# Kernel tuning notes

Measured on AMD Instinct MI355X. Metric: run time of the kernel, lower is better.

Reference implementation:

```python
import jax, jax.numpy as jnp
import numpy as np
from jax import lax

MAX_U = 5
MAX_V = 5
BN_EPS = 1e-5


def _conv(x, w, b, p):
    # NCHW conv with symmetric padding p (torch Conv2d padding=p)
    y = lax.conv_general_dilated(x, w, (1, 1), [(p, p), (p, p)],
                                 dimension_numbers=('NCHW', 'OIHW', 'NCHW'))
    return y + b[None, :, None, None]


def _branch(x, w3, b3, w5, b5, w7, b7):
    a3 = jax.nn.relu(_conv(x, w3, b3, 1))
    a5 = jax.nn.relu(_conv(jnp.concatenate([a3, x], 1), w5, b5, 2))
    a7 = jax.nn.relu(_conv(jnp.concatenate([a5, x], 1), w7, b7, 3))
    return jnp.concatenate([a3, a5, a7], 1)  # [B, 448, H, W]


def _dct_basis(n, kmax, dtype):
    # orthonormal DCT-II basis rows for frequencies u < kmax: [kmax, n]
    i = jnp.arange(n, dtype=dtype)
    u = jnp.arange(kmax, dtype=dtype)
    basis = jnp.cos(jnp.pi * (2.0 * i[None, :] + 1.0) * u[:, None] / (2.0 * n))
    scale = jnp.where(u == 0, jnp.sqrt(1.0 / n), jnp.sqrt(2.0 / n))
    return basis * scale[:, None]


def setup_inputs() -> dict:
    key = jax.random.key(0)
    ks = iter(jax.random.split(key, 64))

    def w(shape, s=0.05):
        return (jax.random.normal(next(ks), shape, jnp.float32) * s)

    cin = 3  # input_channels per group (x has 2*cin = 6 channels)
    inp = {"x": jax.random.normal(next(ks), (16, 6, 64, 64), jnp.float32)}
    for g in (1, 2):
        for b in (1, 2):
            inp[f"g{g}b{b}c3_w"] = w((64, cin, 3, 3))
            inp[f"g{g}b{b}c3_b"] = w((64,))
            inp[f"g{g}b{b}c5_w"] = w((128, 64 + cin, 5, 5))
            inp[f"g{g}b{b}c5_b"] = w((128,))
            inp[f"g{g}b{b}c7_w"] = w((256, 128 + cin, 7, 7))
            inp[f"g{g}b{b}c7_b"] = w((256,))
    inp["gap_w"] = w((12, 1792)); inp["gap_b"] = w((12,))
    inp["dct_w"] = w((12, 1792)); inp["dct_b"] = w((12,))
    inp["bn_gamma"] = jnp.ones((1792,), jnp.float32)
    inp["bn_beta"] = jnp.zeros((1792,), jnp.float32)
    inp["bn_mean"] = jnp.zeros((1792,), jnp.float32)
    inp["bn_var"] = jnp.ones((1792,), jnp.float32)
    return inp


def reference(x,
              g1b1c3_w, g1b1c3_b, g1b1c5_w, g1b1c5_b, g1b1c7_w, g1b1c7_b,
              g1b2c3_w, g1b2c3_b, g1b2c5_w, g1b2c5_b, g1b2c7_w, g1b2c7_b,
              g2b1c3_w, g2b1c3_b, g2b1c5_w, g2b1c5_b, g2b1c7_w, g2b1c7_b,
              g2b2c3_w, g2b2c3_b, g2b2c5_w, g2b2c5_b, g2b2c7_w, g2b2c7_b,
              gap_w, gap_b, dct_w, dct_b, bn_gamma, bn_beta, bn_mean, bn_var):
    B, C, H, W = x.shape  # C is even (6)
    half = C // 2
    x1, x2 = x[:, :half], x[:, half:]
    out1 = jnp.concatenate([
        _branch(x1, g1b1c3_w, g1b1c3_b, g1b1c5_w, g1b1c5_b, g1b1c7_w, g1b1c7_b),
        _branch(x1, g1b2c3_w, g1b2c3_b, g1b2c5_w, g1b2c5_b, g1b2c7_w, g1b2c7_b)], 1)
    out2 = jnp.concatenate([
        _branch(x2, g2b1c3_w, g2b1c3_b, g2b1c5_w, g2b1c5_b, g2b1c7_w, g2b1c7_b),
        _branch(x2, g2b2c3_w, g2b2c3_b, g2b2c5_w, g2b2c5_b, g2b2c7_w, g2b2c7_b)], 1)
    concat_out = jnp.concatenate([out1, out2], 1)  # [B, 1792, H, W]

    # GAP head
    gap = concat_out.mean((2, 3))  # [B, 1792]
    gap_pred = gap @ gap_w.T + gap_b

    # Batched multi-frequency DCT compression: low-frequency 5x5 block of the
    # 2D DCT-II of each channel, averaged -> one scalar per channel.
    Bh = _dct_basis(H, MAX_U, x.dtype)  # [5, H]
    Bw = _dct_basis(W, MAX_V, x.dtype)  # [5, W]
    coeff = jnp.einsum('bchw,uh,vw->bcuv', concat_out, Bh, Bw)  # [B,1792,5,5]
    dct_feat = coeff.mean((2, 3))  # [B, 1792]

    # BatchNorm1d (inference with running stats); dropout is identity in eval.
    bn = bn_gamma * (dct_feat - bn_mean) / jnp.sqrt(bn_var + BN_EPS) + bn_beta
    dct_pred = bn @ dct_w.T + dct_b
    return gap_pred, dct_pred
```

## Files before the change

kernel.cpp:

```cpp
#include <hip/hip_runtime.h>
#include <hip/hip_bf16.h>
#include <math.h>

#define HW 64
#define NPIX 4096
#define NB 16
#define NCH 1792
#define PW 72
#define PROWS 70
#define PLANE (PROWS * PW)

typedef __bf16 bf16;
typedef __bf16 bf16x8 __attribute__((ext_vector_type(8)));
typedef float f32x4 __attribute__((ext_vector_type(4)));

struct PtrQuad { const float* p[4]; };

constexpr size_t W3SZ = 9 * 1 * 64 * 32;
constexpr size_t W5SZ = 25 * 3 * 128 * 32;
constexpr size_t W7SZ = 49 * 5 * 256 * 32;
constexpr size_t WBR  = W3SZ + W5SZ + W7SZ;
constexpr size_t PLE  = (size_t)PLANE * 8;

__global__ __launch_bounds__(256) void init_kernel(float* __restrict__ gap_sum,
                                                   float* __restrict__ dct_sum,
                                                   float* __restrict__ dctw) {
    int tid = blockIdx.x * 256 + threadIdx.x;
    if (tid < NB * NCH) { gap_sum[tid] = 0.f; dct_sum[tid] = 0.f; }
    if (blockIdx.x == 0 && threadIdx.x < HW) {
        int i = threadIdx.x;
        float s = 0.f;
        for (int u = 0; u < 5; ++u) {
            float scale = (u == 0) ? 0.125f : 0.17677669529663687f;
            s += cosf(3.14159265358979323846f * (2.f * i + 1.f) * u / 128.f) * scale;
        }
        dctw[i] = s * 0.2f;
    }
}

__global__ __launch_bounds__(256) void zero_kernel(float4* __restrict__ p, long n) {
    long i = (long)blockIdx.x * 256 + threadIdx.x;
    long stride = (long)gridDim.x * 256;
    for (; i < n; i += stride) p[i] = float4{0.f, 0.f, 0.f, 0.f};
}

__global__ __launch_bounds__(256) void prep_x_kernel(const float* __restrict__ x,
                                                     bf16* __restrict__ xp) {
    int tid = blockIdx.x * 256 + threadIdx.x;
    if (tid >= NB * 2 * NPIX) return;
    int pix = tid & (NPIX - 1);
    int g = (tid >> 12) & 1;
    int b = tid >> 13;
    int h = pix >> 6, w = pix & 63;
    size_t base = ((size_t)(b * 2 + g) * 4) * PLE + ((size_t)(h + 3) * PW + (w + 3)) * 8;
    for (int c = 0; c < 3; ++c)
        xp[base + c] = (bf16)x[((size_t)(b * 6 + g * 3 + c)) * NPIX + pix];
}

template <int K, int CHUNKS, int CIN_ACT, int COUT>
__global__ __launch_bounds__(256) void prep_w_all(PtrQuad src, bf16* __restrict__ dst) {
    constexpr int CIN = CIN_ACT + 3;
    constexpr int TOT = K * K * CHUNKS * COUT * 32;
    int tid = blockIdx.x * 256 + threadIdx.x;
    if (tid >= 4 * TOT) return;
    int br = tid / TOT;
    int idx = tid - br * TOT;
    int cc = idx & 31;
    int co = (idx >> 5) % COUT;
    int rest = idx / (32 * COUT);
    int chunk = rest % CHUNKS;
    int ks = rest / CHUNKS;
    int ky = ks / K, kx = ks % K;
    int ci;
    if (chunk < CHUNKS - 1) ci = chunk * 32 + cc;
    else ci = (cc < 3) ? (CIN_ACT + cc) : -1;
    const float* w = src.p[br];
    float v = (ci >= 0) ? w[(((size_t)co * CIN + ci) * K + ky) * K + kx] : 0.f;
    dst[(size_t)br * WBR + idx] = (bf16)v;
}

template <int K, int CHUNKS, int COUT, int NBLK, bool STORE>
__global__ __launch_bounds__(512, 2) void conv_mfma(
    const bf16* __restrict__ act_in,
    const bf16* __restrict__ xpad,
    const bf16* __restrict__ wall, size_t stage_woff,
    PtrQuad biasq,
    bf16* __restrict__ act_out,
    float* __restrict__ gap_sum, float* __restrict__ dct_sum,
    int stage_coff, const float* __restrict__ dctw, int br0)
{
    constexpr int PAD = K / 2;
    constexpr int COFF = 3 - PAD;
    constexpr int HR = 8 + K - 1;
    constexpr int RH = HR / 2;
    constexpr int UN = RH * PW;
    constexpr int NI = (UN + 63) / 64;
    constexpr int BUFU = 4 * HR * PW;
    constexpr int ACT_CHUNKS = CHUNKS - 1;
    constexpr int WN = NBLK / 32;
    constexpr int CW = CHUNKS * COUT * 32;
    constexpr int OPL = COUT / 8;

    __shared__ __align__(16) bf16 s_in[2 * BUFU * 8];

    const int tid = threadIdx.x;
    const int lane = tid & 63;
    const int wv = tid >> 6;
    const int wavem = wv >> 1;
    const int wn = wv & 1;
    const int q = lane >> 4;
    const int ln = lane & 15;
    const int sseg = wv >> 1;
    const int shalf = wv & 1;

    const int bz = blockIdx.z;
    const int b = bz & 15;
    const int lbr = bz >> 4;
    const int br = br0 + lbr;
    const int g = br >> 1;

    const int o0 = blockIdx.x * 8;
    const int prow0 = o0 + COFF;
    const int n0 = blockIdx.y * NBLK + wn * (NBLK / 2);

    const bf16* wrep = wall + (size_t)br * WBR + stage_woff;
    const float* bias = biasq.p[br];
    const size_t img = (size_t)(lbr * NB + b);

    int abase[8];
#pragma unroll
    for (int t = 0; t < 8; ++t) {
        int lr = wavem * 2 + (t >> 2);
        int ct = (t & 3) * 16;
        abase[t] = ((q * HR + lr) * PW + ct + ln + COFF) * 8;
    }

    f32x4 acc[8][WN];
#pragma unroll
    for (int t = 0; t < 8; ++t)
#pragma unroll
        for (int u = 0; u < WN; ++u) acc[t][u] = f32x4{0.f, 0.f, 0.f, 0.f};

    auto issue = [&](int chunk, int sel) {
        const bf16* pl;
        if (chunk < ACT_CHUNKS)
            pl = act_in + (img * (ACT_CHUNKS * 4) + chunk * 4 + sseg) * PLE;
        else
            pl = xpad + ((size_t)((b * 2 + g) * 4 + sseg)) * PLE;
        const bf16* gb = pl + (size_t)(prow0 + shalf * RH) * PW * 8;
        const bf16* lb = s_in + ((size_t)sel * BUFU + (sseg * HR + shalf * RH) * PW) * 8;
#pragma unroll
        for (int i = 0; i < NI; ++i) {
            int u = i * 64 + lane;
            if (u < UN)
                __builtin_amdgcn_global_load_lds(
                    (const __attribute__((address_space(1))) void*)(gb + (size_t)u * 8),
                    (__attribute__((address_space(3))) void*)(lb + i * 512),
                    16, 0, 0);
        }
    };

    auto compute = [&](int chunk, int sel) {
        const bf16* buf = s_in + (size_t)sel * BUFU * 8;
        const bf16* wchunk = wrep + ((size_t)chunk * COUT + n0) * 32 + ln * 32 + q * 8;
#pragma unroll 1
        for (int ky = 0; ky < K; ++ky) {
            const bf16* wky = wchunk + (size_t)(ky * K) * CW;
            const int kyoff = ky * PW * 8;
#pragma unroll
            for (int kx = 0; kx < K; ++kx) {
                const bf16* wstep = wky + (size_t)kx * CW;
                bf16x8 bfr[WN];
#pragma unroll
                for (int u = 0; u < WN; ++u)
                    bfr[u] = *(const bf16x8*)(wstep + u * 512);
                const int koff = kyoff + kx * 8;
                bf16x8 afr[8];
#pragma unroll
                for (int t = 0; t < 8; ++t)
                    afr[t] = *(const bf16x8*)(buf + abase[t] + koff);
#pragma unroll
                for (int t = 0; t < 8; ++t)
#pragma unroll
                    for (int u = 0; u < WN; ++u)
                        acc[t][u] = __builtin_amdgcn_mfma_f32_16x16x32_bf16(
                            afr[t], bfr[u], acc[t][u], 0, 0, 0);
            }
        }
    };

    issue(0, 0);
#pragma unroll 1
    for (int c = 0; c < CHUNKS - 1; ++c) {
        issue(c + 1, (c + 1) & 1);
        __builtin_amdgcn_s_waitcnt(0xF70 | NI);
        __builtin_amdgcn_s_barrier();
        compute(c, c & 1);
        __builtin_amdgcn_s_barrier();
    }
    __builtin_amdgcn_s_waitcnt(0xF70);
    __builtin_amdgcn_s_barrier();
    compute(CHUNKS - 1, (CHUNKS - 1) & 1);

    float gsum[WN], dsum[WN], bv[WN];
#pragma unroll
    for (int u = 0; u < WN; ++u) {
        gsum[u] = 0.f; dsum[u] = 0.f;
        bv[u] = bias[n0 + u * 16 + ln];
    }

#pragma unroll
    for (int t = 0; t < 8; ++t) {
        const int lr = wavem * 2 + (t >> 2);
        const int gr = o0 + lr;
        const float wrow = dctw[gr];
        const int ct = (t & 3) * 16;
#pragma unroll
        for (int r = 0; r < 4; ++r) {
            const int gc = ct + q * 4 + r;
            const float wcd = dctw[gc] * wrow;
#pragma unroll
            for (int u = 0; u < WN; ++u) {
                float v = fmaxf(acc[t][u][r] + bv[u], 0.f);
                if constexpr (STORE) {
                    int ch = n0 + u * 16 + ln;
                    act_out[(img * OPL + (ch >> 3)) * PLE +
                            ((size_t)(gr + 3) * PW + (gc + 3)) * 8 + (ch & 7)] = (bf16)v;
                }
                gsum[u] += v;
                dsum[u] = fmaf(v, wcd, dsum[u]);
            }
        }
    }

    const int cb = br * 448 + stage_coff;
#pragma unroll
    for (int u = 0; u < WN; ++u) {
        float gv = gsum[u], dv = dsum[u];
        gv += __shfl_xor(gv, 16, 64); gv += __shfl_xor(gv, 32, 64);
        dv += __shfl_xor(dv, 16, 64); dv += __shfl_xor(dv, 32, 64);
        if (q == 0) {
            int ch = cb + n0 + u * 16 + ln;
            atomicAdd(&gap_sum[b * NCH + ch], gv);
            atomicAdd(&dct_sum[b * NCH + ch], dv);
        }
    }
}

__global__ __launch_bounds__(256) void head_kernel(
    const float* __restrict__ gap_sum, const float* __restrict__ dct_sum,
    const float* __restrict__ gap_w, const float* __restrict__ gap_b,
    const float* __restrict__ dct_w, const float* __restrict__ dct_b,
    const float* __restrict__ gamma, const float* __restrict__ beta,
    const float* __restrict__ mean, const float* __restrict__ var,
    float* __restrict__ out)
{
    const int blk = blockIdx.x;
    const int b = blk / 24;
    const int rem = blk - b * 24;
    const int kind = rem / 12;
    const int i = rem - kind * 12;
    const int tid = threadIdx.x;

    float partial = 0.f;
    if (kind == 0) {
        for (int cc = tid; cc < NCH; cc += 256)
            partial += gap_sum[b * NCH + cc] * (1.f / 4096.f) * gap_w[i * NCH + cc];
    } else {
        for (int cc = tid; cc < NCH; cc += 256) {
            float f = dct_sum[b * NCH + cc];
            f = gamma[cc] * (f - mean[cc]) * rsqrtf(var[cc] + 1e-5f) + beta[cc];
            partial += f * dct_w[i * NCH + cc];
        }
    }
#pragma unroll
    for (int off = 32; off > 0; off >>= 1) partial += __shfl_down(partial, off, 64);
    __shared__ float red[4];
    if ((tid & 63) == 0) red[tid >> 6] = partial;
    __syncthreads();
    if (tid == 0) {
        float tot = red[0] + red[1] + red[2] + red[3];
        tot += (kind == 0 ? gap_b[i] : dct_b[i]);
        out[kind * (NB * 12) + b * 12 + i] = tot;
    }
}

extern "C" void kernel_launch(void* const* d_in, const int* in_sizes, int n_in,
                              void* d_out, int out_size, void* d_ws, size_t ws_size,
                              hipStream_t stream)
{
    const float* x = (const float*)d_in[0];

    float* fws = (float*)d_ws;
    float* dctw    = fws;
    float* gap_sum = fws + 64;
    float* dct_sum = gap_sum + NB * NCH;
    bf16* bws = (bf16*)(dct_sum + NB * NCH);

    const size_t WALL_E = 4 * WBR;
    const size_t XP_E   = (size_t)NB * 2 * 4 * PLE;
    const size_t A3_BR  = (size_t)NB * 8 * PLE;
    const size_t A5_BR  = (size_t)NB * 16 * PLE;

    const size_t fixed_b = 229632 + 2 * (WALL_E + XP_E);
    int nbr = 1;
    if (ws_size >= fixed_b + 2 * 4 * (A3_BR + A5_BR)) nbr = 4;
    else if (ws_size >= fixed_b + 2 * 2 * (A3_BR + A5_BR)) nbr = 2;

    bf16* wall = bws;
    bf16* xp   = wall + WALL_E;
    bf16* a3p  = xp + XP_E;
    bf16* a5p  = a3p + (size_t)nbr * A3_BR;

    hipLaunchKernelGGL(init_kernel, dim3((NB * NCH + 255) / 256), dim3(256), 0, stream,
                       gap_sum, dct_sum, dctw);

    const long zero16 = (long)((XP_E + (size_t)nbr * (A3_BR + A5_BR)) * 2 / 16);
    hipLaunchKernelGGL(zero_kernel, dim3(2048), dim3(256), 0, stream, (float4*)xp, zero16);

    hipLaunchKernelGGL(prep_x_kernel, dim3((NB * 2 * NPIX) / 256), dim3(256), 0, stream, x, xp);

    PtrQuad w3q = {{(const float*)d_in[1], (const float*)d_in[7], (const float*)d_in[13], (const float*)d_in[19]}};
    PtrQuad b3q = {{(const float*)d_in[2], (const float*)d_in[8], (const float*)d_in[14], (const float*)d_in[20]}};
    PtrQuad w5q = {{(const float*)d_in[3], (const float*)d_in[9], (const float*)d_in[15], (const float*)d_in[21]}};
    PtrQuad b5q = {{(const float*)d_in[4], (const float*)d_in[10], (const float*)d_in[16], (const float*)d_in[22]}};
    PtrQuad w7q = {{(const float*)d_in[5], (const float*)d_in[11], (const float*)d_in[17], (const float*)d_in[23]}};
    PtrQuad b7q = {{(const float*)d_in[6], (const float*)d_in[12], (const float*)d_in[18], (const float*)d_in[24]}};

    hipLaunchKernelGGL((prep_w_all<3, 1, 0, 64>), dim3((4 * W3SZ + 255) / 256), dim3(256), 0, stream, w3q, wall);
    hipLaunchKernelGGL((prep_w_all<5, 3, 64, 128>), dim3((4 * W5SZ + 255) / 256), dim3(256), 0, stream, w5q, wall + W3SZ);
    hipLaunchKernelGGL((prep_w_all<7, 5, 128, 256>), dim3((4 * W7SZ + 255) / 256), dim3(256), 0, stream, w7q, wall + W3SZ + W5SZ);

    for (int br0 = 0; br0 < 4; br0 += nbr) {
        hipLaunchKernelGGL((conv_mfma<3, 1, 64, 64, true>), dim3(8, 1, NB * nbr), dim3(512), 0, stream,
                           (const bf16*)nullptr, xp, wall, 0, b3q,
                           a3p, gap_sum, dct_sum, 0, dctw, br0);
        hipLaunchKernelGGL((conv_mfma<5, 3, 128, 128, true>), dim3(8, 1, NB * nbr), dim3(512), 0, stream,
                           a3p, xp, wall, W3SZ, b5q,
                           a5p, gap_sum, dct_sum, 64, dctw, br0);
        hipLaunchKernelGGL((conv_mfma<7, 5, 256, 128, false>), dim3(8, 2, NB * nbr), dim3(512), 0, stream,
                           a5p, xp, wall, W3SZ + W5SZ, b7q,
                           (bf16*)nullptr, gap_sum, dct_sum, 192, dctw, br0);
    }

    hipLaunchKernelGGL(head_kernel, dim3(NB * 24), dim3(256), 0, stream,
                       gap_sum, dct_sum,
                       (const float*)d_in[25], (const float*)d_in[26],
                       (const float*)d_in[27], (const float*)d_in[28],
                       (const float*)d_in[29], (const float*)d_in[30],
                       (const float*)d_in[31], (const float*)d_in[32],
                       (float*)d_out);
}
```

Before: 1.014 ms.

## Shrink conv tiles to 2 rows per block with register-prefetched MFMA operands

Each conv block now covers 2 output rows with 256 threads instead of 8 rows with 512, so the grid has 4x more blocks and each block uses less LDS. The double-buffered async LDS pipeline is replaced by a single buffer loaded between two __syncthreads per chunk. Inside a chunk the loop over K*K filter taps is fully unrolled, and the next tap's A and B fragments are loaded into registers while the current tap's MFMAs run. The smaller tile means more halo rows reloaded per output row and global loads no longer overlap compute across chunks, in exchange for more occupancy and shorter dependency chains.

```diff
diff --git a/kernel.cpp b/kernel.cpp
--- a/kernel.cpp
+++ b/kernel.cpp
@@ -80,7 +80,7 @@
 }
 
 template <int K, int CHUNKS, int COUT, int NBLK, bool STORE>
-__global__ __launch_bounds__(512, 2) void conv_mfma(
+__global__ __launch_bounds__(256, 3) void conv_mfma(
     const bf16* __restrict__ act_in,
     const bf16* __restrict__ xpad,
     const bf16* __restrict__ wall, size_t stage_woff,
@@ -91,17 +91,16 @@
 {
     constexpr int PAD = K / 2;
     constexpr int COFF = 3 - PAD;
-    constexpr int HR = 8 + K - 1;
-    constexpr int RH = HR / 2;
-    constexpr int UN = RH * PW;
+    constexpr int HR = K + 1;
+    constexpr int UN = HR * PW;
     constexpr int NI = (UN + 63) / 64;
-    constexpr int BUFU = 4 * HR * PW;
     constexpr int ACT_CHUNKS = CHUNKS - 1;
     constexpr int WN = NBLK / 32;
     constexpr int CW = CHUNKS * COUT * 32;
+    constexpr int KK = K * K;
     constexpr int OPL = COUT / 8;
 
-    __shared__ __align__(16) bf16 s_in[2 * BUFU * 8];
+    __shared__ __align__(16) bf16 s_in[4 * HR * PW * 8];
 
     const int tid = threadIdx.x;
     const int lane = tid & 63;
@@ -110,8 +109,6 @@
     const int wn = wv & 1;
     const int q = lane >> 4;
     const int ln = lane & 15;
-    const int sseg = wv >> 1;
-    const int shalf = wv & 1;
 
     const int bz = blockIdx.z;
     const int b = bz & 15;
@@ -119,7 +116,7 @@
     const int br = br0 + lbr;
     const int g = br >> 1;
 
-    const int o0 = blockIdx.x * 8;
+    const int o0 = blockIdx.x * 2;
     const int prow0 = o0 + COFF;
     const int n0 = blockIdx.y * NBLK + wn * (NBLK / 2);
 
@@ -127,80 +124,73 @@
     const float* bias = biasq.p[br];
     const size_t img = (size_t)(lbr * NB + b);
 
-    int abase[8];
-#pragma unroll
-    for (int t = 0; t < 8; ++t) {
-        int lr = wavem * 2 + (t >> 2);
-        int ct = (t & 3) * 16;
-        abase[t] = ((q * HR + lr) * PW + ct + ln + COFF) * 8;
-    }
-
-    f32x4 acc[8][WN];
-#pragma unroll
-    for (int t = 0; t < 8; ++t)
+    int abase[4];
+#pragma unroll
+    for (int t = 0; t < 4; ++t)
+        abase[t] = ((q * HR + wavem) * PW + t * 16 + ln + COFF) * 8;
+
+    f32x4 acc[4][WN];
+#pragma unroll
+    for (int t = 0; t < 4; ++t)
 #pragma unroll
         for (int u = 0; u < WN; ++u) acc[t][u] = f32x4{0.f, 0.f, 0.f, 0.f};
 
-    auto issue = [&](int chunk, int sel) {
-        const bf16* pl;
-        if (chunk < ACT_CHUNKS)
-            pl = act_in + (img * (ACT_CHUNKS * 4) + chunk * 4 + sseg) * PLE;
-        else
-            pl = xpad + ((size_t)((b * 2 + g) * 4 + sseg)) * PLE;
-        const bf16* gb = pl + (size_t)(prow0 + shalf * RH) * PW * 8;
-        const bf16* lb = s_in + ((size_t)sel * BUFU + (sseg * HR + shalf * RH) * PW) * 8;
-#pragma unroll
-        for (int i = 0; i < NI; ++i) {
-            int u = i * 64 + lane;
-            if (u < UN)
-                __builtin_amdgcn_global_load_lds(
-                    (const __attribute__((address_space(1))) void*)(gb + (size_t)u * 8),
-                    (__attribute__((address_space(3))) void*)(lb + i * 512),
-                    16, 0, 0);
-        }
-    };
-
-    auto compute = [&](int chunk, int sel) {
-        const bf16* buf = s_in + (size_t)sel * BUFU * 8;
+    const bf16* xsrc = xpad + ((size_t)((b * 2 + g) * 4 + wv)) * PLE;
+
+#pragma unroll 1
+    for (int chunk = 0; chunk < CHUNKS; ++chunk) {
+        __syncthreads();
+        {
+            const bf16* pl = (chunk < ACT_CHUNKS)
+                ? act_in + (img * (ACT_CHUNKS * 4) + chunk * 4 + wv) * PLE
+                : xsrc;
+            const bf16* gb = pl + (size_t)prow0 * PW * 8;
+            bf16* lb = s_in + (size_t)wv * HR * PW * 8;
+#pragma unroll
+            for (int i = 0; i < NI; ++i) {
+                int u = i * 64 + lane;
+                if (UN % 64 == 0 || u < UN)
+                    __builtin_amdgcn_global_load_lds(
+                        (const __attribute__((address_space(1))) void*)(gb + (size_t)u * 8),
+                        (__attribute__((address_space(3))) void*)(lb + i * 512),
+                        16, 0, 0);
+            }
+        }
+        __syncthreads();
+
         const bf16* wchunk = wrep + ((size_t)chunk * COUT + n0) * 32 + ln * 32 + q * 8;
-#pragma unroll 1
-        for (int ky = 0; ky < K; ++ky) {
-            const bf16* wky = wchunk + (size_t)(ky * K) * CW;
-            const int kyoff = ky * PW * 8;
-#pragma unroll
-            for (int kx = 0; kx < K; ++kx) {
-                const bf16* wstep = wky + (size_t)kx * CW;
-                bf16x8 bfr[WN];
+
+        bf16x8 A0[4], A1[4], B0[WN], B1[WN];
+#pragma unroll
+        for (int t = 0; t < 4; ++t) A0[t] = *(const bf16x8*)(s_in + abase[t]);
+#pragma unroll
+        for (int u = 0; u < WN; ++u) B0[u] = *(const bf16x8*)(wchunk + u * 512);
+
+#pragma unroll
+        for (int tp = 0; tp < KK; ++tp) {
+            bf16x8* Ac = (tp & 1) ? A1 : A0;
+            bf16x8* Bc = (tp & 1) ? B1 : B0;
+            bf16x8* An = (tp & 1) ? A0 : A1;
+            bf16x8* Bn = (tp & 1) ? B0 : B1;
+            if (tp + 1 < KK) {
+                const int ky = (tp + 1) / K, kx = (tp + 1) - ky * K;
+                const int koff = (ky * PW + kx) * 8;
+#pragma unroll
+                for (int t = 0; t < 4; ++t)
+                    An[t] = *(const bf16x8*)(s_in + abase[t] + koff);
+                const bf16* wstep = wchunk + (size_t)(tp + 1) * CW;
 #pragma unroll
                 for (int u = 0; u < WN; ++u)
-                    bfr[u] = *(const bf16x8*)(wstep + u * 512);
-                const int koff = kyoff + kx * 8;
-                bf16x8 afr[8];
-#pragma unroll
-                for (int t = 0; t < 8; ++t)
-                    afr[t] = *(const bf16x8*)(buf + abase[t] + koff);
-#pragma unroll
-                for (int t = 0; t < 8; ++t)
-#pragma unroll
-                    for (int u = 0; u < WN; ++u)
-                        acc[t][u] = __builtin_amdgcn_mfma_f32_16x16x32_bf16(
-                            afr[t], bfr[u], acc[t][u], 0, 0, 0);
+                    Bn[u] = *(const bf16x8*)(wstep + u * 512);
             }
-        }
-    };
-
-    issue(0, 0);
-#pragma unroll 1
-    for (int c = 0; c < CHUNKS - 1; ++c) {
-        issue(c + 1, (c + 1) & 1);
-        __builtin_amdgcn_s_waitcnt(0xF70 | NI);
-        __builtin_amdgcn_s_barrier();
-        compute(c, c & 1);
-        __builtin_amdgcn_s_barrier();
-    }
-    __builtin_amdgcn_s_waitcnt(0xF70);
-    __builtin_amdgcn_s_barrier();
-    compute(CHUNKS - 1, (CHUNKS - 1) & 1);
+#pragma unroll
+            for (int t = 0; t < 4; ++t)
+#pragma unroll
+                for (int u = 0; u < WN; ++u)
+                    acc[t][u] = __builtin_amdgcn_mfma_f32_16x16x32_bf16(
+                        Ac[t], Bc[u], acc[t][u], 0, 0, 0);
+        }
+    }
 
     float gsum[WN], dsum[WN], bv[WN];
 #pragma unroll
@@ -209,15 +199,14 @@
         bv[u] = bias[n0 + u * 16 + ln];
     }
 
-#pragma unroll
-    for (int t = 0; t < 8; ++t) {
-        const int lr = wavem * 2 + (t >> 2);
-        const int gr = o0 + lr;
-        const float wrow = dctw[gr];
-        const int ct = (t & 3) * 16;
+    const int gr = o0 + wavem;
+    const float wrow = dctw[gr];
+
+#pragma unroll
+    for (int t = 0; t < 4; ++t) {
 #pragma unroll
         for (int r = 0; r < 4; ++r) {
-            const int gc = ct + q * 4 + r;
+            const int gc = t * 16 + q * 4 + r;
             const float wcd = dctw[gc] * wrow;
 #pragma unroll
             for (int u = 0; u < WN; ++u) {
@@ -332,13 +321,13 @@
     hipLaunchKernelGGL((prep_w_all<7, 5, 128, 256>), dim3((4 * W7SZ + 255) / 256), dim3(256), 0, stream, w7q, wall + W3SZ + W5SZ);
 
     for (int br0 = 0; br0 < 4; br0 += nbr) {
-        hipLaunchKernelGGL((conv_mfma<3, 1, 64, 64, true>), dim3(8, 1, NB * nbr), dim3(512), 0, stream,
+        hipLaunchKernelGGL((conv_mfma<3, 1, 64, 64, true>), dim3(32, 1, NB * nbr), dim3(256), 0, stream,
                            (const bf16*)nullptr, xp, wall, 0, b3q,
                            a3p, gap_sum, dct_sum, 0, dctw, br0);
-        hipLaunchKernelGGL((conv_mfma<5, 3, 128, 128, true>), dim3(8, 1, NB * nbr), dim3(512), 0, stream,
+        hipLaunchKernelGGL((conv_mfma<5, 3, 128, 128, true>), dim3(32, 1, NB * nbr), dim3(256), 0, stream,
                            a3p, xp, wall, W3SZ, b5q,
                            a5p, gap_sum, dct_sum, 64, dctw, br0);
-        hipLaunchKernelGGL((conv_mfma<7, 5, 256, 128, false>), dim3(8, 2, NB * nbr), dim3(512), 0, stream,
+        hipLaunchKernelGGL((conv_mfma<7, 5, 256, 128, false>), dim3(32, 2, NB * nbr), dim3(256), 0, stream,
                            a5p, xp, wall, W3SZ + W5SZ, b7q,
                            (bf16*)nullptr, gap_sum, dct_sum, 192, dctw, br0);
     }
```

Result: slower. 1.333 ms (+31.4%).
